# Kernel optimization log

Hardware: AMD Instinct MI355X
Metric: run time of the kernel (lower is better)

Reference implementation:

```python
import jax, jax.numpy as jnp
import numpy as np

B, T, D = 2, 2048, 4096
H, HKV, HD = 32, 8, 128
N_REP = H // HKV
THETA = 500000.0


def _rope(x, cos, sin):
    # x: [B, T, h, HD]; cos/sin: [T, HD//2]
    xr = x.reshape(*x.shape[:-1], HD // 2, 2)
    x0, x1 = xr[..., 0], xr[..., 1]
    c = cos[None, :, None, :]
    s = sin[None, :, None, :]
    o0 = x0 * c - x1 * s
    o1 = x0 * s + x1 * c
    return jnp.stack([o0, o1], axis=-1).reshape(x.shape)


def setup_inputs() -> dict:
    key = jax.random.key(0)
    ks = jax.random.split(key, 8)
    x = jax.random.normal(ks[0], (B, T, D), dtype=jnp.float32)
    # true Llama RoPE angles
    inv_freq = 1.0 / (THETA ** (np.arange(0, HD, 2, dtype=np.float32) / HD))
    ang = np.outer(np.arange(T, dtype=np.float32), inv_freq)  # [T, HD//2]
    freqs_cos = jnp.asarray(np.cos(ang), dtype=jnp.float32)
    freqs_sin = jnp.asarray(np.sin(ang), dtype=jnp.float32)
    mask = jnp.zeros((T, T), dtype=jnp.float32)  # accepted but unused (as in source)
    cache_k = jnp.zeros((B, T, HKV, HD), dtype=jnp.float32)
    cache_v = jnp.zeros((B, T, HKV, HD), dtype=jnp.float32)
    sc = 0.02
    wq = jax.random.normal(ks[1], (D, H * HD), dtype=jnp.float32) * sc
    wk = jax.random.normal(ks[2], (D, HKV * HD), dtype=jnp.float32) * sc
    wv = jax.random.normal(ks[3], (D, HKV * HD), dtype=jnp.float32) * sc
    wo = jax.random.normal(ks[4], (H * HD, D), dtype=jnp.float32) * sc
    return {"x": x, "freqs_cos": freqs_cos, "freqs_sin": freqs_sin, "mask": mask,
            "cache_k": cache_k, "cache_v": cache_v,
            "wq": wq, "wk": wk, "wv": wv, "wo": wo, "start_pos": 0}


def reference(x, freqs_cos, freqs_sin, mask, cache_k, cache_v, wq, wk, wv, wo, start_pos):
    b, t, _ = x.shape
    q = (x @ wq).reshape(b, t, H, HD)
    k = (x @ wk).reshape(b, t, HKV, HD)
    v = (x @ wv).reshape(b, t, HKV, HD)
    q = _rope(q, freqs_cos, freqs_sin)
    k = _rope(k, freqs_cos, freqs_sin)
    # KV-cache write
    cache_k = jax.lax.dynamic_update_slice(cache_k, k, (0, start_pos, 0, 0))
    cache_v = jax.lax.dynamic_update_slice(cache_v, v, (0, start_pos, 0, 0))
    s_len = start_pos + t
    keys = jnp.repeat(cache_k[:, :s_len], N_REP, axis=2)    # [B, S, H, HD]
    values = jnp.repeat(cache_v[:, :s_len], N_REP, axis=2)  # [B, S, H, HD]
    # per-head scaled dot-product attention (vectorized over heads)
    scores = jnp.einsum('bthd,bshd->bhts', q, keys) / jnp.sqrt(jnp.float32(HD))
    probs = jax.nn.softmax(scores, axis=-1)  # mask is NOT applied in the source forward
    out = jnp.einsum('bhts,bshd->bthd', probs, values).reshape(b, t, H * HD)
    return out @ wo
```

## Files before the change

### kernel.cpp

```cpp
#include <hip/hip_runtime.h>

typedef unsigned short u16;
typedef unsigned int   u32;
typedef __attribute__((ext_vector_type(2))) unsigned int u32x2;
typedef __attribute__((ext_vector_type(4))) float f32x4;
typedef __attribute__((ext_vector_type(8))) short s16x8;
typedef __attribute__((ext_vector_type(4))) _Float16 f16x4;
typedef __attribute__((ext_vector_type(8))) _Float16 f16x8;

#define B_   2
#define T_   2048
#define D_   4096
#define H_   32
#define HKV_ 8
#define HD_  128
#define NQKV 6144
#define M_   (B_*T_)

__device__ __forceinline__ u16 f2bf(float f){
  u32 u = __float_as_uint(f);
  u += 0x7fffu + ((u >> 16) & 1u);
  return (u16)(u >> 16);
}
__device__ __forceinline__ float bf2f(u16 h){
  return __uint_as_float(((u32)h) << 16);
}
__device__ __forceinline__ void gload16(const void* g, void* l){
  __builtin_amdgcn_global_load_lds(
      (const __attribute__((address_space(1))) u32*)g,
      (__attribute__((address_space(3))) u32*)l, 16, 0, 0);
}

__global__ void k_convert_x(const float* __restrict__ in, u16* __restrict__ out){
  int i = blockIdx.x * 256 + threadIdx.x;
  float4 v = reinterpret_cast<const float4*>(in)[i];
  u32 lo = (u32)f2bf(v.x) | ((u32)f2bf(v.y) << 16);
  u32 hi = (u32)f2bf(v.z) | ((u32)f2bf(v.w) << 16);
  u32x2 p; p.x = lo; p.y = hi;
  reinterpret_cast<u32x2*>(out)[i] = p;
}

__global__ void k_transpose_w(const float* __restrict__ in, u16* __restrict__ out,
                              int K, int N){
  __shared__ float tile[32][33];
  int n0 = blockIdx.x * 32, k0 = blockIdx.y * 32;
  int tx = threadIdx.x, ty = threadIdx.y;
  #pragma unroll
  for (int i = ty; i < 32; i += 8)
    tile[i][tx] = in[(size_t)(k0 + i) * N + n0 + tx];
  __syncthreads();
  #pragma unroll
  for (int i = ty; i < 32; i += 8)
    out[(size_t)(n0 + i) * K + k0 + tx] = f2bf(tile[tx][i]);
}

template<int OUT_F32>
__global__ __launch_bounds__(256, 2) void k_gemm(
    const u16* __restrict__ A, const u16* __restrict__ Bt,
    void* __restrict__ Cv, int M, int N, int K)
{
  __shared__ __attribute__((aligned(16))) unsigned char smem[32768];
  unsigned char* As = smem;
  unsigned char* Bs = smem + 16384;
  const int tid = threadIdx.x;
  const int w = tid >> 6, l = tid & 63;
  const int m0 = blockIdx.y * 128, n0 = blockIdx.x * 128;
  const int wm = (w >> 1) * 64, wn = (w & 1) * 64;
  f32x4 acc[4][4];
  #pragma unroll
  for (int i = 0; i < 4; i++)
    #pragma unroll
    for (int j = 0; j < 4; j++)
      acc[i][j] = f32x4{0.f, 0.f, 0.f, 0.f};

  const int srcoff = 8 * ((l & 7) ^ ((l >> 3) & 7));
  const int subrow = l >> 3;

  for (int k0 = 0; k0 < K; k0 += 64) {
    if (k0) __syncthreads();
    #pragma unroll
    for (int i = 0; i < 4; i++) {
      int chunk = 4 * w + i;
      int row = chunk * 8 + subrow;
      gload16(A  + (size_t)(m0 + row) * K + k0 + srcoff, As + chunk * 1024);
      gload16(Bt + (size_t)(n0 + row) * K + k0 + srcoff, Bs + chunk * 1024);
    }
    asm volatile("s_waitcnt vmcnt(0)" ::: "memory");
    __syncthreads();
    #pragma unroll
    for (int kk = 0; kk < 2; kk++) {
      s16x8 a[4], b[4];
      const int co = kk * 64 + 16 * (l >> 4);
      #pragma unroll
      for (int mi = 0; mi < 4; mi++) {
        int r = wm + 16 * mi + (l & 15);
        a[mi] = *reinterpret_cast<const s16x8*>(As + r * 128 + (co ^ ((r & 7) << 4)));
      }
      #pragma unroll
      for (int ni = 0; ni < 4; ni++) {
        int r = wn + 16 * ni + (l & 15);
        b[ni] = *reinterpret_cast<const s16x8*>(Bs + r * 128 + (co ^ ((r & 7) << 4)));
      }
      #pragma unroll
      for (int mi = 0; mi < 4; mi++)
        #pragma unroll
        for (int ni = 0; ni < 4; ni++)
          acc[mi][ni] = __builtin_amdgcn_mfma_f32_16x16x32_bf16(a[mi], b[ni], acc[mi][ni], 0, 0, 0);
    }
  }
  const int g = l >> 4, c = l & 15;
  #pragma unroll
  for (int mi = 0; mi < 4; mi++)
    #pragma unroll
    for (int ni = 0; ni < 4; ni++)
      #pragma unroll
      for (int r = 0; r < 4; r++) {
        int m = m0 + wm + 16 * mi + 4 * g + r;
        int n = n0 + wn + 16 * ni + c;
        float v = acc[mi][ni][r];
        if (OUT_F32) reinterpret_cast<float*>(Cv)[(size_t)m * N + n] = v;
        else         reinterpret_cast<u16*>(Cv)[(size_t)m * N + n] = f2bf(v);
      }
}

__global__ void k_rope_q(u16* C1, const float* __restrict__ fc, const float* __restrict__ fs){
  int idx = blockIdx.x * 256 + threadIdx.x;
  int m = idx >> 11, p = idx & 2047;
  int h = p >> 6, i = p & 63;
  int t = m & (T_ - 1);
  u32* ptr = reinterpret_cast<u32*>(C1 + (size_t)m * NQKV + h * HD_ + 2 * i);
  u32 u = *ptr;
  float x0 = __uint_as_float(u << 16);
  float x1 = __uint_as_float(u & 0xffff0000u);
  float cc = fc[t * 64 + i], ss = fs[t * 64 + i];
  float o0 = x0 * cc - x1 * ss;
  float o1 = x0 * ss + x1 * cc;
  *ptr = (u32)f2bf(o0) | ((u32)f2bf(o1) << 16);
}

__global__ void k_rope_k(const u16* __restrict__ C1, const float* __restrict__ fc,
                         const float* __restrict__ fs, unsigned char* __restrict__ Kg){
  int idx = blockIdx.x * 256 + threadIdx.x;
  int m = idx >> 9, p = idx & 511;
  int kh = p >> 6, i = p & 63;
  int b = m >> 11, t = m & (T_ - 1);
  u32 u = *reinterpret_cast<const u32*>(C1 + (size_t)m * NQKV + D_ + kh * HD_ + 2 * i);
  float x0 = __uint_as_float(u << 16);
  float x1 = __uint_as_float(u & 0xffff0000u);
  float cc = fc[t * 64 + i], ss = fs[t * 64 + i];
  float o0 = x0 * cc - x1 * ss;
  float o1 = x0 * ss + x1 * cc;
  u32 packed = (u32)f2bf(o0) | ((u32)f2bf(o1) << 16);
  unsigned char* Kbb = Kg + (size_t)(b * HKV_ + kh) * 524288;
  int swb = (((i >> 2) ^ (t & 7)) << 4) | (4 * (i & 3));
  *reinterpret_cast<u32*>(Kbb + (size_t)t * 256 + swb) = packed;
}

__global__ void k_v_trans(const u16* __restrict__ C1, unsigned char* __restrict__ Vg){
  __shared__ float tile[32][33];
  int bz = blockIdx.z;
  int t0 = blockIdx.x * 32, d0 = blockIdx.y * 32;
  int tx = threadIdx.x, ty = threadIdx.y;
  int b = bz >> 3, kh = bz & 7;
  const u16* src = C1 + (size_t)(b * T_) * NQKV + D_ + HKV_ * HD_ + kh * HD_;
  #pragma unroll
  for (int i = ty; i < 32; i += 8)
    tile[i][tx] = bf2f(src[(size_t)(t0 + i) * NQKV + d0 + tx]);
  __syncthreads();
  unsigned char* Vbb = Vg + (size_t)bz * 524288;
  #pragma unroll
  for (int i = ty; i < 32; i += 8) {
    int d = d0 + i;
    int k = t0 + tx;
    int tt = k >> 6, kv = k & 63;
    int pp = (kv & 0x23) | ((kv & 0x10) >> 2) | ((kv & 0x0C) << 1);
    int swb = (((pp >> 3) ^ (d & 7)) << 4) | (2 * (pp & 7));
    *reinterpret_cast<_Float16*>(Vbb + (size_t)tt * 16384 + d * 128 + swb) =
        (_Float16)tile[tx][i];
  }
}

__global__ __launch_bounds__(256, 2) void k_attn(
    const u16* __restrict__ Q,
    const unsigned char* __restrict__ Kg,
    const unsigned char* __restrict__ Vg,
    u16* __restrict__ Ob)
{
  __shared__ __attribute__((aligned(16))) unsigned char smem[65536];
  const int tid = threadIdx.x;
  const int w = tid >> 6, l = tid & 63;
  const int c = l & 15, g = l >> 4;
  const int q0 = blockIdx.x * 128 + w * 32;
  const int h = blockIdx.y, b = blockIdx.z;
  const int kh = h >> 2;
  const unsigned char* Kb_ = Kg + (size_t)(b * HKV_ + kh) * 524288;
  const unsigned char* Vb_ = Vg + (size_t)(b * HKV_ + kh) * 524288;

  const float SCL2 = 0.08838834764831845f * 1.4426950408889634f;
  const float OFF2 = 14.4269504f;

  s16x8 qf[2][4];
  #pragma unroll
  for (int qt = 0; qt < 2; qt++)
    #pragma unroll
    for (int ci = 0; ci < 4; ci++)
      qf[qt][ci] = *reinterpret_cast<const s16x8*>(
          Q + (size_t)(b * T_ + q0 + 16 * qt + c) * NQKV + h * HD_ + 32 * ci + 8 * g);

  f32x4 o[2][8];
  #pragma unroll
  for (int qt = 0; qt < 2; qt++)
    #pragma unroll
    for (int i = 0; i < 8; i++) o[qt][i] = f32x4{0.f, 0.f, 0.f, 0.f};
  float lsum[2] = {0.f, 0.f};

  auto stage = [&](int bi, int tt) {
    const unsigned char* Ks = Kb_ + (size_t)tt * 16384;
    const unsigned char* Vs = Vb_ + (size_t)tt * 16384;
    unsigned char* Kl = smem + bi * 32768;
    unsigned char* Vl = Kl + 16384;
    #pragma unroll
    for (int i = 0; i < 4; i++) {
      int ch = i * 4 + w;
      gload16(Ks + ch * 1024 + l * 16, Kl + ch * 1024);
      gload16(Vs + ch * 1024 + l * 16, Vl + ch * 1024);
    }
  };

  stage(0, 0);
  asm volatile("s_waitcnt vmcnt(0)" ::: "memory");
  __syncthreads();

  for (int tt = 0; tt < T_ / 64; ++tt) {
    int cur = tt & 1;
    if (tt < T_ / 64 - 1) stage(cur ^ 1, tt + 1);
    const unsigned char* Kl = smem + cur * 32768;
    const unsigned char* Vl = Kl + 16384;

    f32x4 s[4][2];
    #pragma unroll
    for (int mi = 0; mi < 4; mi++)
      #pragma unroll
      for (int qt = 0; qt < 2; qt++) s[mi][qt] = f32x4{0.f, 0.f, 0.f, 0.f};

    #pragma unroll
    for (int mi = 0; mi < 4; mi++) {
      const int row = 16 * mi + c;
      const int sw = (row & 7) << 4;
      s16x8 kf[4];
      #pragma unroll
      for (int ci = 0; ci < 4; ci++)
        kf[ci] = *reinterpret_cast<const s16x8*>(Kl + row * 256 + ((64 * ci + 16 * g) ^ sw));
      #pragma unroll
      for (int qt = 0; qt < 2; qt++)
        #pragma unroll
        for (int ci = 0; ci < 4; ci++)
          s[mi][qt] = __builtin_amdgcn_mfma_f32_16x16x32_bf16(kf[ci], qf[qt][ci], s[mi][qt], 0, 0, 0);
    }

    f16x4 pa[2][4];
    #pragma unroll
    for (int qt = 0; qt < 2; qt++)
      #pragma unroll
      for (int mi = 0; mi < 4; mi++)
        #pragma unroll
        for (int r = 0; r < 4; r++) {
          float p = exp2f(s[mi][qt][r] * SCL2 - OFF2);
          lsum[qt] += p;
          pa[qt][mi][r] = (_Float16)p;
        }

    #pragma unroll
    for (int cp = 0; cp < 2; cp++)
      #pragma unroll
      for (int dc = 0; dc < 8; dc++) {
        const int d = 16 * dc + c;
        f16x8 v8 = *reinterpret_cast<const f16x8*>(
            Vl + d * 128 + ((64 * cp + 16 * g) ^ ((d & 7) << 4)));
        f16x4 lo = {v8[0], v8[1], v8[2], v8[3]};
        f16x4 hi = {v8[4], v8[5], v8[6], v8[7]};
        #pragma unroll
        for (int qt = 0; qt < 2; qt++) {
          o[qt][dc] = __builtin_amdgcn_mfma_f32_16x16x16f16(pa[qt][2 * cp], lo, o[qt][dc], 0, 0, 0);
          o[qt][dc] = __builtin_amdgcn_mfma_f32_16x16x16f16(pa[qt][2 * cp + 1], hi, o[qt][dc], 0, 0, 0);
        }
      }

    asm volatile("s_waitcnt vmcnt(0)" ::: "memory");
    __syncthreads();
  }

  #pragma unroll
  for (int qt = 0; qt < 2; qt++) {
    lsum[qt] += __shfl_xor(lsum[qt], 16);
    lsum[qt] += __shfl_xor(lsum[qt], 32);
  }
  float inv[2][4];
  #pragma unroll
  for (int qt = 0; qt < 2; qt++)
    #pragma unroll
    for (int r = 0; r < 4; r++)
      inv[qt][r] = 1.0f / __shfl(lsum[qt], 4 * g + r, 64);

  #pragma unroll
  for (int qt = 0; qt < 2; qt++) {
    u16* Orow = Ob + (size_t)(b * T_ + q0 + 16 * qt) * D_ + h * HD_;
    #pragma unroll
    for (int dc = 0; dc < 8; dc++)
      #pragma unroll
      for (int r = 0; r < 4; r++)
        Orow[(size_t)(4 * g + r) * D_ + 16 * dc + c] = f2bf(o[qt][dc][r] * inv[qt][r]);
  }
}

extern "C" void kernel_launch(void* const* d_in, const int* in_sizes, int n_in,
                              void* d_out, int out_size, void* d_ws, size_t ws_size,
                              hipStream_t stream)
{
  const float* x  = (const float*)d_in[0];
  const float* fc = (const float*)d_in[1];
  const float* fs = (const float*)d_in[2];
  const float* wq = (const float*)d_in[6];
  const float* wk = (const float*)d_in[7];
  const float* wv = (const float*)d_in[8];
  const float* wo = (const float*)d_in[9];

  unsigned char* w = (unsigned char*)d_ws;
  u16* Xb   = (u16*)(w);
  u16* Wt   = (u16*)(w + 33554432ull);
  u16* Wot  = (u16*)(w + 83886080ull);
  u16* C1   = (u16*)(w + 117440512ull);
  unsigned char* Kg = w + 167772160ull;
  unsigned char* Vg = w + 176160768ull;
  u16* Ob   = (u16*)(w + 184549376ull);

  k_convert_x<<<16384, 256, 0, stream>>>(x, Xb);
  k_transpose_w<<<dim3(128, 128), dim3(32, 8), 0, stream>>>(wq, Wt, D_, D_);
  k_transpose_w<<<dim3(32, 128),  dim3(32, 8), 0, stream>>>(wk, Wt + (size_t)D_ * D_, D_, 1024);
  k_transpose_w<<<dim3(32, 128),  dim3(32, 8), 0, stream>>>(wv, Wt + (size_t)5120 * D_, D_, 1024);
  k_transpose_w<<<dim3(128, 128), dim3(32, 8), 0, stream>>>(wo, Wot, D_, D_);

  k_gemm<0><<<dim3(NQKV / 128, M_ / 128), 256, 0, stream>>>(Xb, Wt, C1, M_, NQKV, D_);

  k_rope_q<<<32768, 256, 0, stream>>>(C1, fc, fs);
  k_rope_k<<<8192, 256, 0, stream>>>(C1, fc, fs, Kg);
  k_v_trans<<<dim3(64, 4, 16), dim3(32, 8), 0, stream>>>(C1, Vg);

  k_attn<<<dim3(T_ / 128, H_, B_), 256, 0, stream>>>(C1, Kg, Vg, Ob);

  k_gemm<1><<<dim3(D_ / 128, M_ / 128), 256, 0, stream>>>(Ob, Wot, d_out, M_, D_, D_);
}
```

Before: 630.7 us.

## Replace GEMM with 256x256-tile double-buffered pipelined kernel and XCD-aware block remap

Replaces the 128x128 single-buffered GEMM with a 512-thread kernel computing 256x256 tiles. Global-to-LDS loads are double-buffered across two 64-wide K stages, with barriers, priority hints and partial vmcnt waits interleaving loads with MFMA work. A flat grid is remapped so consecutive blocks spread across the XCD chiplets. This is meant to hide global load latency and raise data reuse per LDS byte. The cost is 128KB of LDS and more registers, which limits occupancy, and the tile-count remap assumes it divides by 8.

```diff
diff --git a/kernel.cpp b/kernel.cpp
--- a/kernel.cpp
+++ b/kernel.cpp
@@ -54,69 +54,110 @@
     out[(size_t)(n0 + i) * K + k0 + tx] = f2bf(tile[tx][i]);
 }
 
+#define AS_(b) (smem + (b) * 65536)
+#define BS_(b) (smem + (b) * 65536 + 32768)
+#define BARX  asm volatile("s_barrier" ::: "memory")
+#define PRIO1 __builtin_amdgcn_s_setprio(1)
+#define PRIO0 __builtin_amdgcn_s_setprio(0)
+#define VM8   asm volatile("s_waitcnt vmcnt(8)" ::: "memory")
+#define VM0   asm volatile("s_waitcnt vmcnt(0)" ::: "memory")
+#define LGKM0 do { asm volatile("s_waitcnt lgkmcnt(0)" ::: "memory"); \
+                   __builtin_amdgcn_sched_barrier(0); } while (0)
+
+#define STAGE_A(buf, k0_) { \
+  _Pragma("unroll") for (int i2 = 0; i2 < 4; i2++) { \
+    int ch = w * 4 + i2; \
+    gload16(A + (size_t)(m0 + ch * 8 + subrow) * K + (k0_) + srcoff, AS_(buf) + ch * 1024); } }
+#define STAGE_B(buf, k0_) { \
+  _Pragma("unroll") for (int i2 = 0; i2 < 4; i2++) { \
+    int ch = w * 4 + i2; \
+    gload16(Bt + (size_t)(n0 + ch * 8 + subrow) * K + (k0_) + srcoff, BS_(buf) + ch * 1024); } }
+#define RD_A(buf, mih) { \
+  _Pragma("unroll") for (int mi = 0; mi < 4; mi++) { \
+    int row = wr * 128 + (mih) * 64 + 16 * mi + c; \
+    const unsigned char* p = AS_(buf) + row * 128; \
+    int sw = (row & 7) << 4; \
+    af[mi][0] = *(const s16x8*)(p + ((16 * g) ^ sw)); \
+    af[mi][1] = *(const s16x8*)(p + ((64 + 16 * g) ^ sw)); } }
+#define RD_B(buf) { \
+  _Pragma("unroll") for (int ni = 0; ni < 4; ni++) { \
+    int row = wc * 64 + 16 * ni + c; \
+    const unsigned char* p = BS_(buf) + row * 128; \
+    int sw = (row & 7) << 4; \
+    bf[ni][0] = *(const s16x8*)(p + ((16 * g) ^ sw)); \
+    bf[ni][1] = *(const s16x8*)(p + ((64 + 16 * g) ^ sw)); } }
+#define MF(mih, kk) { \
+  _Pragma("unroll") for (int mi = 0; mi < 4; mi++) \
+  _Pragma("unroll") for (int ni = 0; ni < 4; ni++) \
+    acc[(mih) * 4 + mi][ni] = __builtin_amdgcn_mfma_f32_16x16x32_bf16( \
+        af[mi][kk], bf[ni][kk], acc[(mih) * 4 + mi][ni], 0, 0, 0); }
+
 template<int OUT_F32>
-__global__ __launch_bounds__(256, 2) void k_gemm(
+__global__ __launch_bounds__(512, 2) void k_gemm2(
     const u16* __restrict__ A, const u16* __restrict__ Bt,
     void* __restrict__ Cv, int M, int N, int K)
 {
-  __shared__ __attribute__((aligned(16))) unsigned char smem[32768];
-  unsigned char* As = smem;
-  unsigned char* Bs = smem + 16384;
+  __shared__ __attribute__((aligned(16))) unsigned char smem[131072];
   const int tid = threadIdx.x;
   const int w = tid >> 6, l = tid & 63;
-  const int m0 = blockIdx.y * 128, n0 = blockIdx.x * 128;
-  const int wm = (w >> 1) * 64, wn = (w & 1) * 64;
-  f32x4 acc[4][4];
-  #pragma unroll
-  for (int i = 0; i < 4; i++)
+  const int c = l & 15, g = l >> 4;
+  const int wr = w >> 2, wc = w & 3;
+
+  const int nbx = N >> 8;
+  const int nwg = nbx * (M >> 8);
+  const int orig = blockIdx.x;
+  const int id = (orig & 7) * (nwg >> 3) + (orig >> 3);
+  const int m0 = (id / nbx) << 8;
+  const int n0 = (id % nbx) << 8;
+
+  const int srcoff = 8 * ((l & 7) ^ ((l >> 3) & 7));
+  const int subrow = l >> 3;
+
+  f32x4 acc[8][4];
+  #pragma unroll
+  for (int i = 0; i < 8; i++)
     #pragma unroll
     for (int j = 0; j < 4; j++)
       acc[i][j] = f32x4{0.f, 0.f, 0.f, 0.f};
-
-  const int srcoff = 8 * ((l & 7) ^ ((l >> 3) & 7));
-  const int subrow = l >> 3;
-
-  for (int k0 = 0; k0 < K; k0 += 64) {
-    if (k0) __syncthreads();
-    #pragma unroll
-    for (int i = 0; i < 4; i++) {
-      int chunk = 4 * w + i;
-      int row = chunk * 8 + subrow;
-      gload16(A  + (size_t)(m0 + row) * K + k0 + srcoff, As + chunk * 1024);
-      gload16(Bt + (size_t)(n0 + row) * K + k0 + srcoff, Bs + chunk * 1024);
-    }
-    asm volatile("s_waitcnt vmcnt(0)" ::: "memory");
-    __syncthreads();
-    #pragma unroll
-    for (int kk = 0; kk < 2; kk++) {
-      s16x8 a[4], b[4];
-      const int co = kk * 64 + 16 * (l >> 4);
-      #pragma unroll
-      for (int mi = 0; mi < 4; mi++) {
-        int r = wm + 16 * mi + (l & 15);
-        a[mi] = *reinterpret_cast<const s16x8*>(As + r * 128 + (co ^ ((r & 7) << 4)));
-      }
-      #pragma unroll
-      for (int ni = 0; ni < 4; ni++) {
-        int r = wn + 16 * ni + (l & 15);
-        b[ni] = *reinterpret_cast<const s16x8*>(Bs + r * 128 + (co ^ ((r & 7) << 4)));
-      }
-      #pragma unroll
-      for (int mi = 0; mi < 4; mi++)
-        #pragma unroll
-        for (int ni = 0; ni < 4; ni++)
-          acc[mi][ni] = __builtin_amdgcn_mfma_f32_16x16x32_bf16(a[mi], b[ni], acc[mi][ni], 0, 0, 0);
-    }
-  }
-  const int g = l >> 4, c = l & 15;
-  #pragma unroll
-  for (int mi = 0; mi < 4; mi++)
+  s16x8 af[4][2], bf[4][2];
+
+  STAGE_B(0, 0); STAGE_A(0, 0);
+  STAGE_B(1, 64); STAGE_A(1, 64);
+  VM8; BARX;
+
+  const int NT2 = K >> 7;
+  for (int it = 0; it < NT2; ++it) {
+    const int k0 = it << 7;
+    const bool st = (it < NT2 - 1);
+    RD_A(0, 0); RD_B(0);
+    BARX; LGKM0; PRIO1; MF(0, 0); PRIO0; BARX;
+    if (st) STAGE_B(0, k0 + 128);
+    BARX; PRIO1; MF(0, 1); PRIO0; BARX;
+    RD_A(0, 1);
+    BARX; LGKM0; PRIO1; MF(1, 0); PRIO0; BARX;
+    if (st) STAGE_A(0, k0 + 128);
+    BARX; PRIO1; MF(1, 1); PRIO0;
+    if (st) { VM8; } else { VM0; }
+    BARX;
+    RD_A(1, 0); RD_B(1);
+    BARX; LGKM0; PRIO1; MF(0, 0); PRIO0; BARX;
+    if (st) STAGE_B(1, k0 + 192);
+    BARX; PRIO1; MF(0, 1); PRIO0; BARX;
+    RD_A(1, 1);
+    BARX; LGKM0; PRIO1; MF(1, 0); PRIO0; BARX;
+    if (st) STAGE_A(1, k0 + 192);
+    BARX; PRIO1; MF(1, 1); PRIO0;
+    if (st) { VM8; BARX; }
+  }
+
+  #pragma unroll
+  for (int mi = 0; mi < 8; mi++)
     #pragma unroll
     for (int ni = 0; ni < 4; ni++)
       #pragma unroll
       for (int r = 0; r < 4; r++) {
-        int m = m0 + wm + 16 * mi + 4 * g + r;
-        int n = n0 + wn + 16 * ni + c;
+        int m = m0 + wr * 128 + 16 * mi + 4 * g + r;
+        int n = n0 + wc * 64 + 16 * ni + c;
         float v = acc[mi][ni][r];
         if (OUT_F32) reinterpret_cast<float*>(Cv)[(size_t)m * N + n] = v;
         else         reinterpret_cast<u16*>(Cv)[(size_t)m * N + n] = f2bf(v);
@@ -340,7 +381,7 @@
   k_transpose_w<<<dim3(32, 128),  dim3(32, 8), 0, stream>>>(wv, Wt + (size_t)5120 * D_, D_, 1024);
   k_transpose_w<<<dim3(128, 128), dim3(32, 8), 0, stream>>>(wo, Wot, D_, D_);
 
-  k_gemm<0><<<dim3(NQKV / 128, M_ / 128), 256, 0, stream>>>(Xb, Wt, C1, M_, NQKV, D_);
+  k_gemm2<0><<<(NQKV / 256) * (M_ / 256), 512, 0, stream>>>(Xb, Wt, C1, M_, NQKV, D_);
 
   k_rope_q<<<32768, 256, 0, stream>>>(C1, fc, fs);
   k_rope_k<<<8192, 256, 0, stream>>>(C1, fc, fs, Kg);
@@ -348,5 +389,5 @@
 
   k_attn<<<dim3(T_ / 128, H_, B_), 256, 0, stream>>>(C1, Kg, Vg, Ob);
 
-  k_gemm<1><<<dim3(D_ / 128, M_ / 128), 256, 0, stream>>>(Ob, Wot, d_out, M_, D_, D_);
-}
+  k_gemm2<1><<<(D_ / 256) * (M_ / 256), 512, 0, stream>>>(Ob, Wot, d_out, M_, D_, D_);
+}
```

New measurement: 884.6 us. +40.3%, slower.
